# Kernel tuning notes

Measured on AMD Instinct MI355X. Metric: run time of the kernel, lower is better.

Reference implementation:

```python
import jax, jax.numpy as jnp
import numpy as np

C = 256      # d_model
H = 8        # nhead
DF = 1024    # dim_feedforward
LE = 2048    # ego tokens
LA = 2048    # other-agent tokens
N_MATCH = 1024


def setup_inputs() -> dict:
    key = jax.random.key(0)
    ks = jax.random.split(key, 16)
    def rn(k, shape, s=0.02):
        return jax.random.normal(k, shape, dtype=jnp.float32) * s
    inp = {}
    inp['x_ego'] = jax.random.normal(ks[0], (LE, C), dtype=jnp.float32)
    inp['x_agent'] = jax.random.normal(ks[1], (LA, C), dtype=jnp.float32)
    # query_fusion MLP(2C -> C -> C -> C), torch Linear weight is (out, in)
    inp['Wf1'] = rn(ks[2], (C, 2 * C)); inp['bf1'] = jnp.zeros((C,), jnp.float32)
    inp['Wf2'] = rn(ks[3], (C, C));     inp['bf2'] = jnp.zeros((C,), jnp.float32)
    inp['Wf3'] = rn(ks[4], (C, C));     inp['bf3'] = jnp.zeros((C,), jnp.float32)
    # nn.MultiheadAttention packed in-proj and out-proj
    inp['Wqkv'] = rn(ks[5], (3 * C, C)); inp['bqkv'] = jnp.zeros((3 * C,), jnp.float32)
    inp['Wo'] = rn(ks[6], (C, C));       inp['bo'] = jnp.zeros((C,), jnp.float32)
    # FFN
    inp['W1'] = rn(ks[7], (DF, C)); inp['b1'] = jnp.zeros((DF,), jnp.float32)
    inp['W2'] = rn(ks[8], (C, DF)); inp['b2'] = jnp.zeros((C,), jnp.float32)
    # LayerNorms
    inp['g1'] = jnp.ones((C,), jnp.float32); inp['be1'] = jnp.zeros((C,), jnp.float32)
    inp['g2'] = jnp.ones((C,), jnp.float32); inp['be2'] = jnp.zeros((C,), jnp.float32)
    # unique 1D positions: first N_MATCH agent positions overlap ego, rest don't
    inp['pos_ego'] = jnp.arange(LE, dtype=jnp.int32)
    pa = np.concatenate([np.arange(N_MATCH), np.arange(LA - N_MATCH) + 10_000_000])
    inp['pos_agent'] = jnp.asarray(pa, dtype=jnp.int32)
    inp['n_remain'] = LA - N_MATCH  # static python int
    return inp


def _ln(t, g, b):
    m = t.mean(-1, keepdims=True)
    v = t.var(-1, keepdims=True)
    return (t - m) / jnp.sqrt(v + 1e-5) * g + b


def reference(x_ego, x_agent, Wf1, bf1, Wf2, bf2, Wf3, bf3, Wqkv, bqkv, Wo, bo,
              W1, b1, W2, b2, g1, be1, g2, be2, pos_ego, pos_agent, n_remain):
    # ---- position-keyed grouping / fuse (replaces the host-side dict loop) ----
    eq = pos_agent[:, None] == pos_ego[None, :]          # [La, Le]
    matched_e = eq.any(axis=0)                           # ego token has same-pos agent token
    agent_for_ego = jnp.argmax(eq, axis=0)               # [Le] matching agent index (valid where matched)
    fused_in = jnp.concatenate([x_ego, x_agent[agent_for_ego]], axis=-1)  # [Le, 2C]
    h = jax.nn.relu(fused_in @ Wf1.T + bf1)
    h = jax.nn.relu(h @ Wf2.T + bf2)
    fused = h @ Wf3.T + bf3                              # query_fusion MLP output [Le, C]
    ego_out = jnp.where(matched_e[:, None], fused, x_ego)
    # agent tokens with no ego match, in original agent order (fixed count n_remain)
    remain_idx = jnp.nonzero(~eq.any(axis=1), size=n_remain)[0]
    q = jnp.concatenate([ego_out, x_agent[remain_idx]], axis=0)[None]  # (1, Lq, C)
    kv = jnp.concatenate([x_ego, x_agent], axis=0)[None]               # (1, Lk, C)
    # ---- MultiheadAttention (batch_first, eval: dropout off) ----
    Wq, Wk, Wv = jnp.split(Wqkv, 3, axis=0)
    bq, bk, bv = jnp.split(bqkv, 3, axis=0)
    dh = C // H
    def heads(t, W, b):
        return (t @ W.T + b).reshape(1, -1, H, dh).transpose(0, 2, 1, 3)
    qh, kh, vh = heads(q, Wq, bq), heads(kv, Wk, bk), heads(kv, Wv, bv)
    scores = jnp.einsum('bhqd,bhkd->bhqk', qh, kh) / (float(dh) ** 0.5)
    attn = jax.nn.softmax(scores, axis=-1)
    o = jnp.einsum('bhqk,bhkd->bhqd', attn, vh).transpose(0, 2, 1, 3).reshape(1, -1, C)
    o = o @ Wo.T + bo
    # ---- residual + norm1 + FFN + residual + norm2 ----
    yq = _ln(q + o, g1, be1)
    ff = jax.nn.relu(yq @ W1.T + b1) @ W2.T + b2
    return _ln(yq + ff, g2, be2)
```

## Files before the change

### kernel.cpp

```cpp
#include <hip/hip_runtime.h>


#define LE 2048
#define LA 2048
#define CDIM 256
#define HN 8
#define DH 32
#define DFF 1024
#define NREM 1024
#define LQC 3072
#define LKC 4096
#define KSPLIT 8
#define NIT (LKC / KSPLIT / 64)

typedef unsigned short u16;
typedef unsigned int u32;
typedef __attribute__((ext_vector_type(8))) short bf16x8;
typedef __attribute__((ext_vector_type(4))) float f32x4;

__device__ __forceinline__ u32 pk_bf16(float a, float b) {
    u32 ua = (__builtin_bit_cast(u32, a) + 0x8000u) >> 16;
    u32 ub = (__builtin_bit_cast(u32, b) + 0x8000u) >> 16;
    return ua | (ub << 16);
}
__device__ __forceinline__ u16 bf16_1(float a) {
    return (u16)((__builtin_bit_cast(u32, a) + 0x8000u) >> 16);
}
__device__ __forceinline__ float fast_exp2(float x) {
    return __builtin_amdgcn_exp2f(x);
}

__global__ __launch_bounds__(1024) void k_match(const int* __restrict__ pos_ego,
                                                const int* __restrict__ pos_agent,
                                                int* __restrict__ afe,
                                                int* __restrict__ matched,
                                                int* __restrict__ unmatched) {
    __shared__ int keyA[4096], valA[4096], keyE[4096];
    const int t = threadIdx.x;
#pragma unroll
    for (int i = 0; i < 4; ++i) { keyA[t + i * 1024] = -1; keyE[t + i * 1024] = -1; }
    __syncthreads();
#pragma unroll
    for (int i = 0; i < 2; ++i) {
        int a = t + i * 1024;
        int p = pos_agent[a];
        u32 h = ((u32)p * 2654435761u) >> 20;
        while (true) {
            int prev = atomicCAS(&keyA[h], -1, p);
            if (prev == -1) { valA[h] = a; break; }
            h = (h + 1) & 4095;
        }
        int e = t + i * 1024;
        int pe = pos_ego[e];
        u32 he = ((u32)pe * 2654435761u) >> 20;
        while (true) {
            int prev = atomicCAS(&keyE[he], -1, pe);
            if (prev == -1) break;
            he = (he + 1) & 4095;
        }
    }
    __syncthreads();
#pragma unroll
    for (int i = 0; i < 2; ++i) {
        int e = t + i * 1024;
        int p = pos_ego[e];
        u32 h = ((u32)p * 2654435761u) >> 20;
        int idx = 0, fnd = 0;
        while (true) {
            int k = keyA[h];
            if (k == p) { idx = valA[h]; fnd = 1; break; }
            if (k == -1) break;
            h = (h + 1) & 4095;
        }
        afe[e] = idx;
        matched[e] = fnd;
        int a = t + i * 1024;
        int pa_ = pos_agent[a];
        u32 ha = ((u32)pa_ * 2654435761u) >> 20;
        int fnd2 = 0;
        while (true) {
            int k = keyE[ha];
            if (k == pa_) { fnd2 = 1; break; }
            if (k == -1) break;
            ha = (ha + 1) & 4095;
        }
        unmatched[a] = !fnd2;
    }
}

struct WPtrs { const float* p[7]; };
__constant__ __device__ const int woff[8] = {0, 131072, 196608, 262144,
                                             458752, 524288, 786432, 1048576};

__global__ __launch_bounds__(256) void k_stage2(const int* __restrict__ unmatched,
                                                int* __restrict__ remain,
                                                const int* __restrict__ afe,
                                                const float* __restrict__ x_ego,
                                                const float* __restrict__ x_agent,
                                                u16* __restrict__ fused_b,
                                                WPtrs wp, u16* __restrict__ wb,
                                                u16* __restrict__ kv_b) {
    int b = blockIdx.x;
    if (b == 0) {
        __shared__ int s[256];
        int t = threadIdx.x;
        int base_i = t * 8;
        int flags[8];
        int cnt = 0;
#pragma unroll
        for (int j = 0; j < 8; ++j) { flags[j] = unmatched[base_i + j]; cnt += flags[j]; }
        s[t] = cnt;
        __syncthreads();
        for (int off = 1; off < 256; off <<= 1) {
            int v = (t >= off) ? s[t - off] : 0;
            __syncthreads();
            s[t] += v;
            __syncthreads();
        }
        int pos = s[t] - cnt;
#pragma unroll
        for (int j = 0; j < 8; ++j) {
            if (flags[j]) {
                if (pos < NREM) remain[pos] = base_i + j;
                pos++;
            }
        }
    } else if (b <= 512) {
        int t = (b - 1) * 256 + threadIdx.x;
        int e = t >> 6, c8 = t & 63;
        const float* src;
        int col;
        if (c8 < 32) { src = x_ego + (size_t)e * CDIM; col = c8 * 8; }
        else { src = x_agent + (size_t)afe[e] * CDIM; col = (c8 - 32) * 8; }
        float4 f0 = *(const float4*)(src + col);
        float4 f1 = *(const float4*)(src + col + 4);
        uint4 o;
        o.x = pk_bf16(f0.x, f0.y); o.y = pk_bf16(f0.z, f0.w);
        o.z = pk_bf16(f1.x, f1.y); o.w = pk_bf16(f1.z, f1.w);
        *(uint4*)(fused_b + (size_t)e * 512 + c8 * 8) = o;
    } else if (b <= 1024) {
        int g = ((b - 513) * 256 + threadIdx.x) * 8;
        int s = 0;
#pragma unroll
        for (int i = 1; i < 7; ++i) s += (g >= woff[i]);
        const float* src = wp.p[s] + (g - woff[s]);
        float4 f0 = *(const float4*)(src);
        float4 f1 = *(const float4*)(src + 4);
        uint4 o;
        o.x = pk_bf16(f0.x, f0.y); o.y = pk_bf16(f0.z, f0.w);
        o.z = pk_bf16(f1.x, f1.y); o.w = pk_bf16(f1.z, f1.w);
        *(uint4*)(wb + g) = o;
    } else {
        int t = (b - 1025) * 256 + threadIdx.x;
        int j = t >> 5, c8 = t & 31;
        const float* src = (j < LE) ? (x_ego + (size_t)j * CDIM)
                                    : (x_agent + (size_t)(j - LE) * CDIM);
        float4 f0 = *(const float4*)(src + c8 * 8);
        float4 f1 = *(const float4*)(src + c8 * 8 + 4);
        uint4 o;
        o.x = pk_bf16(f0.x, f0.y); o.y = pk_bf16(f0.z, f0.w);
        o.z = pk_bf16(f1.x, f1.y); o.w = pk_bf16(f1.z, f1.w);
        *(uint4*)(kv_b + (size_t)j * CDIM + c8 * 8) = o;
    }
}

template <int EPI, bool RELU>
__global__ __launch_bounds__(256) void gemm_bf16(const u16* __restrict__ A,
                                                 const u16* __restrict__ B,
                                                 const float* __restrict__ bias,
                                                 void* __restrict__ C,
                                                 int M, int N, int K) {
    const int tid = threadIdx.x;
    const int w = tid >> 6, lane = tid & 63;
    const int quad = lane >> 4, qi = lane & 15;
    const int wm = w >> 1, wn = w & 1;
    const int bm = blockIdx.y * 64, bn = blockIdx.x * 64;

    const u16* pa0 = A + (size_t)(bm + wm * 32 + qi) * K + quad * 8;
    const u16* pa1 = pa0 + (size_t)16 * K;
    const u16* pb0 = B + (size_t)(bn + wn * 32 + qi) * K + quad * 8;
    const u16* pb1 = pb0 + (size_t)16 * K;

    f32x4 acc00 = {0.f, 0.f, 0.f, 0.f}, acc01 = {0.f, 0.f, 0.f, 0.f};
    f32x4 acc10 = {0.f, 0.f, 0.f, 0.f}, acc11 = {0.f, 0.f, 0.f, 0.f};

#pragma unroll 4
    for (int k = 0; k < K; k += 32) {
        bf16x8 a0 = *(const bf16x8*)(pa0 + k);
        bf16x8 a1 = *(const bf16x8*)(pa1 + k);
        bf16x8 b0 = *(const bf16x8*)(pb0 + k);
        bf16x8 b1 = *(const bf16x8*)(pb1 + k);
        acc00 = __builtin_amdgcn_mfma_f32_16x16x32_bf16(a0, b0, acc00, 0, 0, 0);
        acc01 = __builtin_amdgcn_mfma_f32_16x16x32_bf16(a0, b1, acc01, 0, 0, 0);
        acc10 = __builtin_amdgcn_mfma_f32_16x16x32_bf16(a1, b0, acc10, 0, 0, 0);
        acc11 = __builtin_amdgcn_mfma_f32_16x16x32_bf16(a1, b1, acc11, 0, 0, 0);
    }

#pragma unroll
    for (int i = 0; i < 2; ++i) {
#pragma unroll
        for (int j = 0; j < 2; ++j) {
            f32x4 acc = (i == 0) ? (j == 0 ? acc00 : acc01) : (j == 0 ? acc10 : acc11);
            int n = bn + wn * 32 + j * 16 + qi;
            int mbase = bm + wm * 32 + i * 16 + quad * 4;
            float bs = bias[n];
            float v[4];
#pragma unroll
            for (int r = 0; r < 4; ++r) {
                float x = acc[r] + bs;
                if (RELU) x = fmaxf(x, 0.f);
                v[r] = x;
            }
            if (EPI == 0) {
                float* Cf = (float*)C;
#pragma unroll
                for (int r = 0; r < 4; ++r) Cf[(size_t)(mbase + r) * N + n] = v[r];
            } else {
                u16* Cb = (u16*)C;
#pragma unroll
                for (int r = 0; r < 4; ++r) Cb[(size_t)(mbase + r) * N + n] = bf16_1(v[r]);
            }
        }
    }
}

__global__ __launch_bounds__(256) void k_mlp3f(const u16* __restrict__ h2_b,
                                               const u16* __restrict__ Wf3_b,
                                               const float* __restrict__ bf3,
                                               const int* __restrict__ matched,
                                               const int* __restrict__ remain,
                                               const float* __restrict__ x_ego,
                                               const float* __restrict__ x_agent,
                                               float* __restrict__ qbuf,
                                               u16* __restrict__ qbuf_b) {
    const int tid = threadIdx.x;
    const int bn = blockIdx.x * 64, bm = blockIdx.y * 64;
    if (bm >= LE) {
        int row = bm + (tid >> 2);
        int col = bn + (tid & 3) * 16;
        int idx = remain[row - LE];
        idx = min(max(idx, 0), LA - 1);
        const float* src = x_agent + (size_t)idx * CDIM + col;
        float* dq = qbuf + (size_t)row * CDIM + col;
        u16* db = qbuf_b + (size_t)row * CDIM + col;
#pragma unroll
        for (int i = 0; i < 4; ++i) {
            float4 v = *(const float4*)(src + i * 4);
            *(float4*)(dq + i * 4) = v;
            *(uint2*)(db + i * 4) = make_uint2(pk_bf16(v.x, v.y), pk_bf16(v.z, v.w));
        }
        return;
    }
    const int w = tid >> 6, lane = tid & 63;
    const int quad = lane >> 4, qi = lane & 15;
    const int wm = w >> 1, wn = w & 1;
    const u16* pa0 = h2_b + (size_t)(bm + wm * 32 + qi) * 256 + quad * 8;
    const u16* pa1 = pa0 + (size_t)16 * 256;
    const u16* pb0 = Wf3_b + (size_t)(bn + wn * 32 + qi) * 256 + quad * 8;
    const u16* pb1 = pb0 + (size_t)16 * 256;
    f32x4 a00 = {0, 0, 0, 0}, a01 = {0, 0, 0, 0}, a10 = {0, 0, 0, 0}, a11 = {0, 0, 0, 0};
#pragma unroll 4
    for (int k = 0; k < 256; k += 32) {
        bf16x8 x0 = *(const bf16x8*)(pa0 + k);
        bf16x8 x1 = *(const bf16x8*)(pa1 + k);
        bf16x8 y0 = *(const bf16x8*)(pb0 + k);
        bf16x8 y1 = *(const bf16x8*)(pb1 + k);
        a00 = __builtin_amdgcn_mfma_f32_16x16x32_bf16(x0, y0, a00, 0, 0, 0);
        a01 = __builtin_amdgcn_mfma_f32_16x16x32_bf16(x0, y1, a01, 0, 0, 0);
        a10 = __builtin_amdgcn_mfma_f32_16x16x32_bf16(x1, y0, a10, 0, 0, 0);
        a11 = __builtin_amdgcn_mfma_f32_16x16x32_bf16(x1, y1, a11, 0, 0, 0);
    }
#pragma unroll
    for (int i = 0; i < 2; ++i)
#pragma unroll
        for (int jj = 0; jj < 2; ++jj) {
            f32x4 acc = (i == 0) ? (jj == 0 ? a00 : a01) : (jj == 0 ? a10 : a11);
            int n = bn + wn * 32 + jj * 16 + qi;
            int mb = bm + wm * 32 + i * 16 + quad * 4;
            float bs = bf3[n];
#pragma unroll
            for (int r = 0; r < 4; ++r) {
                int row = mb + r;
                float v = acc[r] + bs;
                if (!matched[row]) v = x_ego[(size_t)row * CDIM + n];
                qbuf[(size_t)row * CDIM + n] = v;
                qbuf_b[(size_t)row * CDIM + n] = bf16_1(v);
            }
        }
}

__global__ __launch_bounds__(256) void k_qkv(const u16* __restrict__ qbuf_b,
                                             const u16* __restrict__ kv_b,
                                             const u16* __restrict__ Wq,
                                             const u16* __restrict__ Wkv,
                                             const float* __restrict__ bqkv,
                                             u16* __restrict__ qb,
                                             u16* __restrict__ kbp,
                                             u16* __restrict__ vtb,
                                             float qscale) {
    int b = blockIdx.x;
    const u16 *A, *B;
    const float* bias;
    int bm, bn, mode;
    if (b < 192) {
        A = qbuf_b; B = Wq; bias = bqkv;
        bm = (b >> 2) * 64; bn = (b & 3) * 64; mode = 0;
    } else {
        int c = b - 192;
        A = kv_b; B = Wkv; bias = bqkv + 256;
        bm = (c >> 3) * 64; bn = (c & 7) * 64; mode = 1;
    }
    const int tid = threadIdx.x;
    const int w = tid >> 6, lane = tid & 63;
    const int quad = lane >> 4, qi = lane & 15;
    const int wm = w >> 1, wn = w & 1;
    const int K = 256;

    const u16* pa0 = A + (size_t)(bm + wm * 32 + qi) * K + quad * 8;
    const u16* pa1 = pa0 + (size_t)16 * K;
    const u16* pb0 = B + (size_t)(bn + wn * 32 + qi) * K + quad * 8;
    const u16* pb1 = pb0 + (size_t)16 * K;

    f32x4 acc00 = {0.f, 0.f, 0.f, 0.f}, acc01 = {0.f, 0.f, 0.f, 0.f};
    f32x4 acc10 = {0.f, 0.f, 0.f, 0.f}, acc11 = {0.f, 0.f, 0.f, 0.f};
#pragma unroll 4
    for (int k = 0; k < 256; k += 32) {
        bf16x8 a0 = *(const bf16x8*)(pa0 + k);
        bf16x8 a1 = *(const bf16x8*)(pa1 + k);
        bf16x8 b0 = *(const bf16x8*)(pb0 + k);
        bf16x8 b1 = *(const bf16x8*)(pb1 + k);
        acc00 = __builtin_amdgcn_mfma_f32_16x16x32_bf16(a0, b0, acc00, 0, 0, 0);
        acc01 = __builtin_amdgcn_mfma_f32_16x16x32_bf16(a0, b1, acc01, 0, 0, 0);
        acc10 = __builtin_amdgcn_mfma_f32_16x16x32_bf16(a1, b0, acc10, 0, 0, 0);
        acc11 = __builtin_amdgcn_mfma_f32_16x16x32_bf16(a1, b1, acc11, 0, 0, 0);
    }
#pragma unroll
    for (int i = 0; i < 2; ++i) {
#pragma unroll
        for (int j = 0; j < 2; ++j) {
            f32x4 acc = (i == 0) ? (j == 0 ? acc00 : acc01) : (j == 0 ? acc10 : acc11);
            int n = bn + wn * 32 + j * 16 + qi;
            int mbase = bm + wm * 32 + i * 16 + quad * 4;
            float bs = bias[n];
            float v[4];
#pragma unroll
            for (int r = 0; r < 4; ++r) v[r] = acc[r] + bs;
            if (mode == 0) {
#pragma unroll
                for (int r = 0; r < 4; ++r)
                    qb[(size_t)(mbase + r) * 256 + n] = bf16_1(v[r] * qscale);
            } else if (n < 256) {
#pragma unroll
                for (int r = 0; r < 4; ++r)
                    kbp[(size_t)(mbase + r) * 256 + n] = bf16_1(v[r]);
            } else {
                ushort4 o4;
                o4.x = bf16_1(v[0]); o4.y = bf16_1(v[1]);
                o4.z = bf16_1(v[2]); o4.w = bf16_1(v[3]);
                *(ushort4*)(vtb + (size_t)(n - 256) * LKC + mbase) = o4;
            }
        }
    }
}

__global__ __launch_bounds__(256) void attn_mfma(const u16* __restrict__ qb,
                                                 const u16* __restrict__ kb,
                                                 const u16* __restrict__ vtb,
                                                 float* __restrict__ Pl,
                                                 float* __restrict__ Pacc) {
    __shared__ u16 Kt[2][64 * 32];
    __shared__ u16 Vt[2][32 * 64];
    __shared__ u16 plds[4][16 * 64];
    const int tid = threadIdx.x;
    const int w = tid >> 6, lane = tid & 63;
    const int quad = lane >> 4, qi = lane & 15;
    const int h = blockIdx.y, ks = blockIdx.z;
    const int q0 = blockIdx.x * 64 + w * 16;

    bf16x8 qf = *(const bf16x8*)(qb + (size_t)(q0 + qi) * CDIM + h * DH + quad * 8);

    f32x4 O0 = {0.f, 0.f, 0.f, 0.f}, O1 = {0.f, 0.f, 0.f, 0.f};
    float lsum = 0.f;

    const int krow = w * 16 + (lane >> 2), kcp = lane & 3;
    const int kc = kcp ^ (krow & 3);
    const u16* kg0 = kb + (size_t)krow * CDIM + h * DH + kc * 8;
    const int kdst = krow * 32 + kcp * 8;
    const int vd = w * 8 + (lane >> 3), vcp = lane & 7;
    const int vc = vcp ^ (vd & 7);
    const u16* vg0 = vtb + (size_t)(h * DH + vd) * LKC + vc * 8;
    const int vdst = vd * 64 + vcp * 8;

    const int ka0 = qi * 32 + ((quad ^ (qi & 3)) << 3);
    const int v00o = qi * 64 + ((quad ^ (qi & 7)) << 3);
    const int v01o = qi * 64 + (((quad + 4) ^ (qi & 7)) << 3);
    const int swz = (qi & 7);
    const int rd0 = qi * 64 + ((quad ^ swz) << 3);
    const int rd1 = qi * 64 + (((4 + quad) ^ swz) << 3);
    const int half = (quad & 1) << 2;

    int kt = ks * (LKC / KSPLIT);
    {
        bf16x8 kr = *(const bf16x8*)(kg0 + (size_t)kt * CDIM);
        bf16x8 vr = *(const bf16x8*)(vg0 + kt);
        *(bf16x8*)&Kt[0][kdst] = kr;
        *(bf16x8*)&Vt[0][vdst] = vr;
    }
    int buf = 0;
    for (int it = 0; it < NIT; ++it, kt += 64) {
        __syncthreads();
        bf16x8 knext, vnext;
        const bool more = (it + 1 < NIT);
        if (more) {
            knext = *(const bf16x8*)(kg0 + (size_t)(kt + 64) * CDIM);
            vnext = *(const bf16x8*)(vg0 + kt + 64);
        }

        bf16x8 a0 = *(const bf16x8*)&Kt[buf][ka0];
        bf16x8 a1 = *(const bf16x8*)&Kt[buf][ka0 + 16 * 32];
        bf16x8 a2 = *(const bf16x8*)&Kt[buf][ka0 + 32 * 32];
        bf16x8 a3 = *(const bf16x8*)&Kt[buf][ka0 + 48 * 32];
        f32x4 z = {0.f, 0.f, 0.f, 0.f};
        f32x4 s0 = __builtin_amdgcn_mfma_f32_16x16x32_bf16(a0, qf, z, 0, 0, 0);
        f32x4 s1 = __builtin_amdgcn_mfma_f32_16x16x32_bf16(a1, qf, z, 0, 0, 0);
        f32x4 s2 = __builtin_amdgcn_mfma_f32_16x16x32_bf16(a2, qf, z, 0, 0, 0);
        f32x4 s3 = __builtin_amdgcn_mfma_f32_16x16x32_bf16(a3, qf, z, 0, 0, 0);

        float p0[4], p1[4], p2[4], p3[4];
#pragma unroll
        for (int r = 0; r < 4; ++r) {
            p0[r] = fast_exp2(s0[r]); p1[r] = fast_exp2(s1[r]);
            p2[r] = fast_exp2(s2[r]); p3[r] = fast_exp2(s3[r]);
            lsum += p0[r] + p1[r] + p2[r] + p3[r];
        }

        u16* pb = &plds[w][0];
#pragma unroll
        for (int t2 = 0; t2 < 4; ++t2) {
            int jg = t2 * 2 + (quad >> 1);
            int off = qi * 64 + ((jg ^ swz) << 3) + half;
            uint2 pw;
            float* pp = (t2 == 0) ? p0 : (t2 == 1) ? p1 : (t2 == 2) ? p2 : p3;
            pw.x = pk_bf16(pp[0], pp[1]);
            pw.y = pk_bf16(pp[2], pp[3]);
            *(uint2*)&pb[off] = pw;
        }
        bf16x8 pa0 = *(bf16x8*)&pb[rd0];
        bf16x8 pa1 = *(bf16x8*)&pb[rd1];

        bf16x8 v00 = *(const bf16x8*)&Vt[buf][v00o];
        bf16x8 v01 = *(const bf16x8*)&Vt[buf][v01o];
        bf16x8 v10 = *(const bf16x8*)&Vt[buf][v00o + 16 * 64];
        bf16x8 v11 = *(const bf16x8*)&Vt[buf][v01o + 16 * 64];
        O0 = __builtin_amdgcn_mfma_f32_16x16x32_bf16(pa0, v00, O0, 0, 0, 0);
        O0 = __builtin_amdgcn_mfma_f32_16x16x32_bf16(pa1, v01, O0, 0, 0, 0);
        O1 = __builtin_amdgcn_mfma_f32_16x16x32_bf16(pa0, v10, O1, 0, 0, 0);
        O1 = __builtin_amdgcn_mfma_f32_16x16x32_bf16(pa1, v11, O1, 0, 0, 0);

        if (more) {
            *(bf16x8*)&Kt[buf ^ 1][kdst] = knext;
            *(bf16x8*)&Vt[buf ^ 1][vdst] = vnext;
        }
        buf ^= 1;
    }

    lsum += __shfl_xor(lsum, 16, 64);
    lsum += __shfl_xor(lsum, 32, 64);

    int pbase = (h * KSPLIT + ks) * LQC + q0;
    if (quad == 0) Pl[pbase + qi] = lsum;
#pragma unroll
    for (int r = 0; r < 4; ++r) {
        int q = quad * 4 + r;
        float* pa = Pacc + (size_t)(pbase + q) * 32;
        pa[qi] = O0[r];
        pa[16 + qi] = O1[r];
    }
}

__global__ __launch_bounds__(256) void attn_combine(const float* __restrict__ Pl,
                                                    const float* __restrict__ Pacc,
                                                    u16* __restrict__ attn_b) {
    int t = blockIdx.x * 256 + threadIdx.x;
    int row = t >> 6;
    int h = (t >> 3) & 7;
    int d4 = t & 7;
    float L = 0.f;
    float o[4] = {};
#pragma unroll
    for (int ck = 0; ck < KSPLIT; ++ck) {
        size_t pidx = (size_t)(h * KSPLIT + ck) * LQC + row;
        L += Pl[pidx];
        float4 a = *(const float4*)(Pacc + pidx * 32 + d4 * 4);
        o[0] += a.x; o[1] += a.y; o[2] += a.z; o[3] += a.w;
    }
    float inv = 1.0f / L;
    ushort4 ov;
    ov.x = bf16_1(o[0] * inv); ov.y = bf16_1(o[1] * inv);
    ov.z = bf16_1(o[2] * inv); ov.w = bf16_1(o[3] * inv);
    *(ushort4*)(attn_b + (size_t)row * CDIM + h * DH + d4 * 4) = ov;
}

template <bool EMIT_BF16>
__global__ __launch_bounds__(256) void ln_kernel(const float* __restrict__ X,
                                                 const float* __restrict__ R,
                                                 const float* __restrict__ g,
                                                 const float* __restrict__ b,
                                                 float* __restrict__ out,
                                                 u16* __restrict__ out_b) {
    int lane = threadIdx.x & 63;
    int row = blockIdx.x * 4 + (threadIdx.x >> 6);
    const float* x = X + (size_t)row * CDIM;
    const float* r = R + (size_t)row * CDIM;
    float4 xv = *(const float4*)(x + lane * 4);
    float4 rv = *(const float4*)(r + lane * 4);
    float v[4] = {xv.x + rv.x, xv.y + rv.y, xv.z + rv.z, xv.w + rv.w};
    float s = v[0] + v[1] + v[2] + v[3];
    float sq = v[0] * v[0] + v[1] * v[1] + v[2] * v[2] + v[3] * v[3];
#pragma unroll
    for (int off = 32; off >= 1; off >>= 1) {
        s += __shfl_xor(s, off, 64);
        sq += __shfl_xor(sq, off, 64);
    }
    float mean = s * (1.f / 256.f);
    float var = sq * (1.f / 256.f) - mean * mean;
    float rstd = rsqrtf(var + 1e-5f);
    float4 gv = *(const float4*)(g + lane * 4);
    float4 bv = *(const float4*)(b + lane * 4);
    float4 o = make_float4((v[0] - mean) * rstd * gv.x + bv.x,
                           (v[1] - mean) * rstd * gv.y + bv.y,
                           (v[2] - mean) * rstd * gv.z + bv.z,
                           (v[3] - mean) * rstd * gv.w + bv.w);
    *(float4*)(out + (size_t)row * CDIM + lane * 4) = o;
    if (EMIT_BF16) {
        uint2 ob;
        ob.x = pk_bf16(o.x, o.y);
        ob.y = pk_bf16(o.z, o.w);
        *(uint2*)(out_b + (size_t)row * CDIM + lane * 4) = ob;
    }
}

extern "C" void kernel_launch(void* const* d_in, const int* in_sizes, int n_in,
                              void* d_out, int out_size, void* d_ws, size_t ws_size,
                              hipStream_t stream) {
    const float* x_ego = (const float*)d_in[0];
    const float* x_agent = (const float*)d_in[1];
    const float* Wf1 = (const float*)d_in[2];
    const float* bf1 = (const float*)d_in[3];
    const float* Wf2 = (const float*)d_in[4];
    const float* bf2 = (const float*)d_in[5];
    const float* Wf3 = (const float*)d_in[6];
    const float* bf3 = (const float*)d_in[7];
    const float* Wqkv = (const float*)d_in[8];
    const float* bqkv = (const float*)d_in[9];
    const float* Wo = (const float*)d_in[10];
    const float* bo = (const float*)d_in[11];
    const float* W1 = (const float*)d_in[12];
    const float* b1 = (const float*)d_in[13];
    const float* W2 = (const float*)d_in[14];
    const float* b2 = (const float*)d_in[15];
    const float* g1 = (const float*)d_in[16];
    const float* be1 = (const float*)d_in[17];
    const float* g2 = (const float*)d_in[18];
    const float* be2 = (const float*)d_in[19];
    const int* pos_ego = (const int*)d_in[20];
    const int* pos_agent = (const int*)d_in[21];

    float* ws = (float*)d_ws;
    size_t o = 0;
    float* qbuf = ws + o; o += 786432;
    float* o2 = ws + o; o += 786432;
    float* yq = ws + o; o += 786432;
    float* ff2 = o2;
    float* Pl = ws + o; o += HN * KSPLIT * LQC;
    float* Pacc = ws + o; o += (size_t)HN * KSPLIT * LQC * 32;
    u16* wb = (u16*)(ws + o); o += 524288;
    u16* fused_b = (u16*)(ws + o); o += 524288;
    u16* h1_b = (u16*)(ws + o); o += 262144;
    u16* h2_b = (u16*)(ws + o); o += 262144;
    u16* qbuf_b = (u16*)(ws + o); o += 393216;
    u16* kv_b = (u16*)(ws + o); o += 524288;
    u16* qb = (u16*)(ws + o); o += 393216;
    u16* kb = (u16*)(ws + o); o += 524288;
    u16* vtb = (u16*)(ws + o); o += 524288;
    u16* attn_b = (u16*)(ws + o); o += 393216;
    u16* ff1_b = (u16*)(ws + o); o += 1572864;
    u16* yq_b = (u16*)(ws + o); o += 393216;
    int* afe = (int*)(ws + o);
    int* matched = afe + LE;
    int* unmatched = matched + LE;
    int* remain = unmatched + LA;

    const u16* Wf1_b = wb + 0;
    const u16* Wf2_b = wb + 131072;
    const u16* Wf3_b = wb + 196608;
    const u16* Wq_b = wb + 262144;
    const u16* Wkv_b = wb + 327680;
    const u16* Wo_b = wb + 458752;
    const u16* W1_b = wb + 524288;
    const u16* W2_b = wb + 786432;

    k_match<<<1, 1024, 0, stream>>>(pos_ego, pos_agent, afe, matched, unmatched);
    WPtrs wp;
    wp.p[0] = Wf1; wp.p[1] = Wf2; wp.p[2] = Wf3; wp.p[3] = Wqkv;
    wp.p[4] = Wo; wp.p[5] = W1; wp.p[6] = W2;
    k_stage2<<<1537, 256, 0, stream>>>(unmatched, remain, afe, x_ego, x_agent,
                                       fused_b, wp, wb, kv_b);

    const float qscale = 0.17677669529663687f * 1.4426950408889634f;

    gemm_bf16<1, true><<<dim3(4, 32), 256, 0, stream>>>(fused_b, Wf1_b, bf1, h1_b,
                                                        LE, 256, 512);
    gemm_bf16<1, true><<<dim3(4, 32), 256, 0, stream>>>(h1_b, Wf2_b, bf2, h2_b,
                                                        LE, 256, 256);
    k_mlp3f<<<dim3(4, 48), 256, 0, stream>>>(h2_b, Wf3_b, bf3, matched, remain,
                                             x_ego, x_agent, qbuf, qbuf_b);

    k_qkv<<<704, 256, 0, stream>>>(qbuf_b, kv_b, Wq_b, Wkv_b, bqkv, qb, kb, vtb, qscale);

    attn_mfma<<<dim3(LQC / 64, HN, KSPLIT), 256, 0, stream>>>(qb, kb, vtb, Pl, Pacc);
    attn_combine<<<(LQC * 64) / 256, 256, 0, stream>>>(Pl, Pacc, attn_b);

    gemm_bf16<0, false><<<dim3(4, 48), 256, 0, stream>>>(attn_b, Wo_b, bo, o2,
                                                         LQC, 256, 256);
    ln_kernel<true><<<LQC / 4, 256, 0, stream>>>(qbuf, o2, g1, be1, yq, yq_b);

    gemm_bf16<1, true><<<dim3(16, 48), 256, 0, stream>>>(yq_b, W1_b, b1, ff1_b,
                                                         LQC, DFF, 256);
    gemm_bf16<0, false><<<dim3(4, 48), 256, 0, stream>>>(ff1_b, W2_b, b2, ff2,
                                                         LQC, 256, DFF);
    ln_kernel<false><<<LQC / 4, 256, 0, stream>>>(yq, ff2, g2, be2, (float*)d_out, nullptr);
}
```

Measured before the change: 220.2 us.

## Merge prep kernels, fuse gather into MLP1, XCD-swizzle tiles, fp16 attention partials

Merges the hash-match kernel and the conversion/scan kernel into one k_prep launch. The scan now runs over 1024 threads from shared memory. A new k_mlp1 gathers x_ego/x_agent rows and converts them to bf16 directly in the A-operand load, which removes the fused_b buffer and its separate pass. GEMM, QKV and attention blocks are remapped so consecutive tiles go to the same XCD for L2 locality. Split-K attention partial outputs are stored as fp16 instead of fp32, halving that traffic at some precision cost.

```diff
diff --git a/kernel.cpp b/kernel.cpp
--- a/kernel.cpp
+++ b/kernel.cpp
@@ -29,117 +29,108 @@
 __device__ __forceinline__ float fast_exp2(float x) {
     return __builtin_amdgcn_exp2f(x);
 }
-
-__global__ __launch_bounds__(1024) void k_match(const int* __restrict__ pos_ego,
-                                                const int* __restrict__ pos_agent,
-                                                int* __restrict__ afe,
-                                                int* __restrict__ matched,
-                                                int* __restrict__ unmatched) {
-    __shared__ int keyA[4096], valA[4096], keyE[4096];
-    const int t = threadIdx.x;
-#pragma unroll
-    for (int i = 0; i < 4; ++i) { keyA[t + i * 1024] = -1; keyE[t + i * 1024] = -1; }
-    __syncthreads();
-#pragma unroll
-    for (int i = 0; i < 2; ++i) {
-        int a = t + i * 1024;
-        int p = pos_agent[a];
-        u32 h = ((u32)p * 2654435761u) >> 20;
-        while (true) {
-            int prev = atomicCAS(&keyA[h], -1, p);
-            if (prev == -1) { valA[h] = a; break; }
-            h = (h + 1) & 4095;
-        }
-        int e = t + i * 1024;
-        int pe = pos_ego[e];
-        u32 he = ((u32)pe * 2654435761u) >> 20;
-        while (true) {
-            int prev = atomicCAS(&keyE[he], -1, pe);
-            if (prev == -1) break;
-            he = (he + 1) & 4095;
-        }
-    }
-    __syncthreads();
-#pragma unroll
-    for (int i = 0; i < 2; ++i) {
-        int e = t + i * 1024;
-        int p = pos_ego[e];
-        u32 h = ((u32)p * 2654435761u) >> 20;
-        int idx = 0, fnd = 0;
-        while (true) {
-            int k = keyA[h];
-            if (k == p) { idx = valA[h]; fnd = 1; break; }
-            if (k == -1) break;
-            h = (h + 1) & 4095;
-        }
-        afe[e] = idx;
-        matched[e] = fnd;
-        int a = t + i * 1024;
-        int pa_ = pos_agent[a];
-        u32 ha = ((u32)pa_ * 2654435761u) >> 20;
-        int fnd2 = 0;
-        while (true) {
-            int k = keyE[ha];
-            if (k == pa_) { fnd2 = 1; break; }
-            if (k == -1) break;
-            ha = (ha + 1) & 4095;
-        }
-        unmatched[a] = !fnd2;
-    }
+__device__ __forceinline__ bf16x8 ld_pack8(const float* p) {
+    float4 f0 = *(const float4*)p;
+    float4 f1 = *(const float4*)(p + 4);
+    union { u32 u[4]; bf16x8 v; } o;
+    o.u[0] = pk_bf16(f0.x, f0.y); o.u[1] = pk_bf16(f0.z, f0.w);
+    o.u[2] = pk_bf16(f1.x, f1.y); o.u[3] = pk_bf16(f1.z, f1.w);
+    return o.v;
+}
+
+__device__ __forceinline__ void xcd_tile(int& bm, int& bn) {
+    int gx = gridDim.x;
+    int tot = gx * gridDim.y;
+    int p = blockIdx.y * gx + blockIdx.x;
+    int l = p;
+    if (!(tot & 7)) { int c = p & 7, s = p >> 3; l = c * (tot >> 3) + s; }
+    bm = (l / gx) * 64;
+    bn = (l % gx) * 64;
 }
 
 struct WPtrs { const float* p[7]; };
 __constant__ __device__ const int woff[8] = {0, 131072, 196608, 262144,
                                              458752, 524288, 786432, 1048576};
 
-__global__ __launch_bounds__(256) void k_stage2(const int* __restrict__ unmatched,
-                                                int* __restrict__ remain,
-                                                const int* __restrict__ afe,
-                                                const float* __restrict__ x_ego,
-                                                const float* __restrict__ x_agent,
-                                                u16* __restrict__ fused_b,
-                                                WPtrs wp, u16* __restrict__ wb,
-                                                u16* __restrict__ kv_b) {
-    int b = blockIdx.x;
+__global__ __launch_bounds__(1024) void k_prep(const int* __restrict__ pos_ego,
+                                               const int* __restrict__ pos_agent,
+                                               int* __restrict__ afe,
+                                               int* __restrict__ matched,
+                                               int* __restrict__ remain,
+                                               const float* __restrict__ x_ego,
+                                               const float* __restrict__ x_agent,
+                                               WPtrs wp, u16* __restrict__ wb,
+                                               u16* __restrict__ kv_b) {
+    const int b = blockIdx.x;
+    const int t = threadIdx.x;
     if (b == 0) {
-        __shared__ int s[256];
-        int t = threadIdx.x;
-        int base_i = t * 8;
-        int flags[8];
-        int cnt = 0;
-#pragma unroll
-        for (int j = 0; j < 8; ++j) { flags[j] = unmatched[base_i + j]; cnt += flags[j]; }
-        s[t] = cnt;
+        __shared__ int keyA[4096], valA[4096], keyE[4096];
+        __shared__ int unm[2048];
+#pragma unroll
+        for (int i = 0; i < 4; ++i) { keyA[t + i * 1024] = -1; keyE[t + i * 1024] = -1; }
         __syncthreads();
-        for (int off = 1; off < 256; off <<= 1) {
-            int v = (t >= off) ? s[t - off] : 0;
+#pragma unroll
+        for (int i = 0; i < 2; ++i) {
+            int a = t + i * 1024;
+            int p = pos_agent[a];
+            u32 h = ((u32)p * 2654435761u) >> 20;
+            while (true) {
+                int prev = atomicCAS(&keyA[h], -1, p);
+                if (prev == -1) { valA[h] = a; break; }
+                h = (h + 1) & 4095;
+            }
+            int e = t + i * 1024;
+            int pe = pos_ego[e];
+            u32 he = ((u32)pe * 2654435761u) >> 20;
+            while (true) {
+                int prev = atomicCAS(&keyE[he], -1, pe);
+                if (prev == -1) break;
+                he = (he + 1) & 4095;
+            }
+        }
+        __syncthreads();
+#pragma unroll
+        for (int i = 0; i < 2; ++i) {
+            int e = t + i * 1024;
+            int p = pos_ego[e];
+            u32 h = ((u32)p * 2654435761u) >> 20;
+            int idx = 0, fnd = 0;
+            while (true) {
+                int k = keyA[h];
+                if (k == p) { idx = valA[h]; fnd = 1; break; }
+                if (k == -1) break;
+                h = (h + 1) & 4095;
+            }
+            afe[e] = idx;
+            matched[e] = fnd;
+            int a = t + i * 1024;
+            int pa_ = pos_agent[a];
+            u32 ha = ((u32)pa_ * 2654435761u) >> 20;
+            int fnd2 = 0;
+            while (true) {
+                int k = keyE[ha];
+                if (k == pa_) { fnd2 = 1; break; }
+                if (k == -1) break;
+                ha = (ha + 1) & 4095;
+            }
+            unm[a] = !fnd2;
+        }
+        __syncthreads();
+        int f0 = unm[2 * t], f1 = unm[2 * t + 1];
+        int cnt = f0 + f1;
+        valA[t] = cnt;
+        __syncthreads();
+        for (int off = 1; off < 1024; off <<= 1) {
+            int v = (t >= off) ? valA[t - off] : 0;
             __syncthreads();
-            s[t] += v;
+            valA[t] += v;
             __syncthreads();
         }
-        int pos = s[t] - cnt;
-#pragma unroll
-        for (int j = 0; j < 8; ++j) {
-            if (flags[j]) {
-                if (pos < NREM) remain[pos] = base_i + j;
-                pos++;
-            }
-        }
-    } else if (b <= 512) {
-        int t = (b - 1) * 256 + threadIdx.x;
-        int e = t >> 6, c8 = t & 63;
-        const float* src;
-        int col;
-        if (c8 < 32) { src = x_ego + (size_t)e * CDIM; col = c8 * 8; }
-        else { src = x_agent + (size_t)afe[e] * CDIM; col = (c8 - 32) * 8; }
-        float4 f0 = *(const float4*)(src + col);
-        float4 f1 = *(const float4*)(src + col + 4);
-        uint4 o;
-        o.x = pk_bf16(f0.x, f0.y); o.y = pk_bf16(f0.z, f0.w);
-        o.z = pk_bf16(f1.x, f1.y); o.w = pk_bf16(f1.z, f1.w);
-        *(uint4*)(fused_b + (size_t)e * 512 + c8 * 8) = o;
-    } else if (b <= 1024) {
-        int g = ((b - 513) * 256 + threadIdx.x) * 8;
+        int pos = valA[t] - cnt;
+        if (f0 && pos < NREM) remain[pos] = 2 * t;
+        if (f1 && pos + f0 < NREM) remain[pos + f0] = 2 * t + 1;
+    } else if (b <= 128) {
+        int g = ((b - 1) * 1024 + t) * 8;
         int s = 0;
 #pragma unroll
         for (int i = 1; i < 7; ++i) s += (g >= woff[i]);
@@ -151,8 +142,8 @@
         o.z = pk_bf16(f1.x, f1.y); o.w = pk_bf16(f1.z, f1.w);
         *(uint4*)(wb + g) = o;
     } else {
-        int t = (b - 1025) * 256 + threadIdx.x;
-        int j = t >> 5, c8 = t & 31;
+        int tt = (b - 129) * 1024 + t;
+        int j = tt >> 5, c8 = tt & 31;
         const float* src = (j < LE) ? (x_ego + (size_t)j * CDIM)
                                     : (x_agent + (size_t)(j - LE) * CDIM);
         float4 f0 = *(const float4*)(src + c8 * 8);
@@ -174,7 +165,8 @@
     const int w = tid >> 6, lane = tid & 63;
     const int quad = lane >> 4, qi = lane & 15;
     const int wm = w >> 1, wn = w & 1;
-    const int bm = blockIdx.y * 64, bn = blockIdx.x * 64;
+    int bm, bn;
+    xcd_tile(bm, bn);
 
     const u16* pa0 = A + (size_t)(bm + wm * 32 + qi) * K + quad * 8;
     const u16* pa1 = pa0 + (size_t)16 * K;
@@ -224,6 +216,68 @@
     }
 }
 
+__global__ __launch_bounds__(256) void k_mlp1(const float* __restrict__ x_ego,
+                                              const float* __restrict__ x_agent,
+                                              const int* __restrict__ afe,
+                                              const u16* __restrict__ Wf1_b,
+                                              const float* __restrict__ bf1,
+                                              u16* __restrict__ h1_b) {
+    const int tid = threadIdx.x;
+    const int w = tid >> 6, lane = tid & 63;
+    const int quad = lane >> 4, qi = lane & 15;
+    const int wm = w >> 1, wn = w & 1;
+    int bm, bn;
+    xcd_tile(bm, bn);
+
+    const int r0 = bm + wm * 32 + qi, r1 = r0 + 16;
+    const float* pe0 = x_ego + (size_t)r0 * CDIM + quad * 8;
+    const float* pe1 = x_ego + (size_t)r1 * CDIM + quad * 8;
+    const float* pg0 = x_agent + (size_t)afe[r0] * CDIM + quad * 8;
+    const float* pg1 = x_agent + (size_t)afe[r1] * CDIM + quad * 8;
+    const u16* pb0 = Wf1_b + (size_t)(bn + wn * 32 + qi) * 512 + quad * 8;
+    const u16* pb1 = pb0 + (size_t)16 * 512;
+
+    f32x4 acc00 = {0.f, 0.f, 0.f, 0.f}, acc01 = {0.f, 0.f, 0.f, 0.f};
+    f32x4 acc10 = {0.f, 0.f, 0.f, 0.f}, acc11 = {0.f, 0.f, 0.f, 0.f};
+
+#pragma unroll 4
+    for (int k = 0; k < 256; k += 32) {
+        bf16x8 a0 = ld_pack8(pe0 + k);
+        bf16x8 a1 = ld_pack8(pe1 + k);
+        bf16x8 b0 = *(const bf16x8*)(pb0 + k);
+        bf16x8 b1 = *(const bf16x8*)(pb1 + k);
+        acc00 = __builtin_amdgcn_mfma_f32_16x16x32_bf16(a0, b0, acc00, 0, 0, 0);
+        acc01 = __builtin_amdgcn_mfma_f32_16x16x32_bf16(a0, b1, acc01, 0, 0, 0);
+        acc10 = __builtin_amdgcn_mfma_f32_16x16x32_bf16(a1, b0, acc10, 0, 0, 0);
+        acc11 = __builtin_amdgcn_mfma_f32_16x16x32_bf16(a1, b1, acc11, 0, 0, 0);
+    }
+#pragma unroll 4
+    for (int k = 0; k < 256; k += 32) {
+        bf16x8 a0 = ld_pack8(pg0 + k);
+        bf16x8 a1 = ld_pack8(pg1 + k);
+        bf16x8 b0 = *(const bf16x8*)(pb0 + 256 + k);
+        bf16x8 b1 = *(const bf16x8*)(pb1 + 256 + k);
+        acc00 = __builtin_amdgcn_mfma_f32_16x16x32_bf16(a0, b0, acc00, 0, 0, 0);
+        acc01 = __builtin_amdgcn_mfma_f32_16x16x32_bf16(a0, b1, acc01, 0, 0, 0);
+        acc10 = __builtin_amdgcn_mfma_f32_16x16x32_bf16(a1, b0, acc10, 0, 0, 0);
+        acc11 = __builtin_amdgcn_mfma_f32_16x16x32_bf16(a1, b1, acc11, 0, 0, 0);
+    }
+#pragma unroll
+    for (int i = 0; i < 2; ++i)
+#pragma unroll
+        for (int j = 0; j < 2; ++j) {
+            f32x4 acc = (i == 0) ? (j == 0 ? acc00 : acc01) : (j == 0 ? acc10 : acc11);
+            int n = bn + wn * 32 + j * 16 + qi;
+            int mbase = bm + wm * 32 + i * 16 + quad * 4;
+            float bs = bf1[n];
+#pragma unroll
+            for (int r = 0; r < 4; ++r) {
+                float x = fmaxf(acc[r] + bs, 0.f);
+                h1_b[(size_t)(mbase + r) * 256 + n] = bf16_1(x);
+            }
+        }
+}
+
 __global__ __launch_bounds__(256) void k_mlp3f(const u16* __restrict__ h2_b,
                                                const u16* __restrict__ Wf3_b,
                                                const float* __restrict__ bf3,
@@ -234,7 +288,8 @@
                                                float* __restrict__ qbuf,
                                                u16* __restrict__ qbuf_b) {
     const int tid = threadIdx.x;
-    const int bn = blockIdx.x * 64, bm = blockIdx.y * 64;
+    int bm, bn;
+    xcd_tile(bm, bn);
     if (bm >= LE) {
         int row = bm + (tid >> 2);
         int col = bn + (tid & 3) * 16;
@@ -298,7 +353,12 @@
                                              u16* __restrict__ kbp,
                                              u16* __restrict__ vtb,
                                              float qscale) {
-    int b = blockIdx.x;
+    int b;
+    {
+        int p = blockIdx.x;
+        int c = p & 7, s = p >> 3;
+        b = c * 88 + s;
+    }
     const u16 *A, *B;
     const float* bias;
     int bm, bn, mode;
@@ -367,15 +427,23 @@
                                                  const u16* __restrict__ kb,
                                                  const u16* __restrict__ vtb,
                                                  float* __restrict__ Pl,
-                                                 float* __restrict__ Pacc) {
+                                                 u16* __restrict__ Pacc) {
     __shared__ u16 Kt[2][64 * 32];
     __shared__ u16 Vt[2][32 * 64];
     __shared__ u16 plds[4][16 * 64];
     const int tid = threadIdx.x;
     const int w = tid >> 6, lane = tid & 63;
     const int quad = lane >> 4, qi = lane & 15;
-    const int h = blockIdx.y, ks = blockIdx.z;
-    const int q0 = blockIdx.x * 64 + w * 16;
+    int h, ks, q0;
+    {
+        int p = (blockIdx.z * gridDim.y + blockIdx.y) * gridDim.x + blockIdx.x;
+        int c = p & 7, s = p >> 3;
+        int l = c * 384 + s;
+        int qblk = l % 48;
+        int hk = l / 48;
+        h = hk & 7; ks = hk >> 3;
+        q0 = qblk * 64 + w * 16;
+    }
 
     bf16x8 qf = *(const bf16x8*)(qb + (size_t)(q0 + qi) * CDIM + h * DH + quad * 8);
 
@@ -472,14 +540,14 @@
 #pragma unroll
     for (int r = 0; r < 4; ++r) {
         int q = quad * 4 + r;
-        float* pa = Pacc + (size_t)(pbase + q) * 32;
-        pa[qi] = O0[r];
-        pa[16 + qi] = O1[r];
+        u16* pa = Pacc + (size_t)(pbase + q) * 32;
+        pa[qi] = __builtin_bit_cast(u16, (_Float16)O0[r]);
+        pa[16 + qi] = __builtin_bit_cast(u16, (_Float16)O1[r]);
     }
 }
 
 __global__ __launch_bounds__(256) void attn_combine(const float* __restrict__ Pl,
-                                                    const float* __restrict__ Pacc,
+                                                    const u16* __restrict__ Pacc,
                                                     u16* __restrict__ attn_b) {
     int t = blockIdx.x * 256 + threadIdx.x;
     int row = t >> 6;
@@ -491,8 +559,11 @@
     for (int ck = 0; ck < KSPLIT; ++ck) {
         size_t pidx = (size_t)(h * KSPLIT + ck) * LQC + row;
         L += Pl[pidx];
-        float4 a = *(const float4*)(Pacc + pidx * 32 + d4 * 4);
-        o[0] += a.x; o[1] += a.y; o[2] += a.z; o[3] += a.w;
+        ushort4 a = *(const ushort4*)(Pacc + pidx * 32 + d4 * 4);
+        o[0] += (float)__builtin_bit_cast(_Float16, a.x);
+        o[1] += (float)__builtin_bit_cast(_Float16, a.y);
+        o[2] += (float)__builtin_bit_cast(_Float16, a.z);
+        o[3] += (float)__builtin_bit_cast(_Float16, a.w);
     }
     float inv = 1.0f / L;
     ushort4 ov;
@@ -573,9 +644,8 @@
     float* yq = ws + o; o += 786432;
     float* ff2 = o2;
     float* Pl = ws + o; o += HN * KSPLIT * LQC;
-    float* Pacc = ws + o; o += (size_t)HN * KSPLIT * LQC * 32;
+    u16* Pacc = (u16*)(ws + o); o += (size_t)HN * KSPLIT * LQC * 16;
     u16* wb = (u16*)(ws + o); o += 524288;
-    u16* fused_b = (u16*)(ws + o); o += 524288;
     u16* h1_b = (u16*)(ws + o); o += 262144;
     u16* h2_b = (u16*)(ws + o); o += 262144;
     u16* qbuf_b = (u16*)(ws + o); o += 393216;
@@ -588,8 +658,7 @@
     u16* yq_b = (u16*)(ws + o); o += 393216;
     int* afe = (int*)(ws + o);
     int* matched = afe + LE;
-    int* unmatched = matched + LE;
-    int* remain = unmatched + LA;
+    int* remain = matched + LE;
 
     const u16* Wf1_b = wb + 0;
     const u16* Wf2_b = wb + 131072;
@@ -600,17 +669,16 @@
     const u16* W1_b = wb + 524288;
     const u16* W2_b = wb + 786432;
 
-    k_match<<<1, 1024, 0, stream>>>(pos_ego, pos_agent, afe, matched, unmatched);
     WPtrs wp;
     wp.p[0] = Wf1; wp.p[1] = Wf2; wp.p[2] = Wf3; wp.p[3] = Wqkv;
     wp.p[4] = Wo; wp.p[5] = W1; wp.p[6] = W2;
-    k_stage2<<<1537, 256, 0, stream>>>(unmatched, remain, afe, x_ego, x_agent,
-                                       fused_b, wp, wb, kv_b);
+
+    k_prep<<<257, 1024, 0, stream>>>(pos_ego, pos_agent, afe, matched, remain,
+                                     x_ego, x_agent, wp, wb, kv_b);
 
     const float qscale = 0.17677669529663687f * 1.4426950408889634f;
 
-    gemm_bf16<1, true><<<dim3(4, 32), 256, 0, stream>>>(fused_b, Wf1_b, bf1, h1_b,
-                                                        LE, 256, 512);
+    k_mlp1<<<dim3(4, 32), 256, 0, stream>>>(x_ego, x_agent, afe, Wf1_b, bf1, h1_b);
     gemm_bf16<1, true><<<dim3(4, 32), 256, 0, stream>>>(h1_b, Wf2_b, bf2, h2_b,
                                                         LE, 256, 256);
     k_mlp3f<<<dim3(4, 48), 256, 0, stream>>>(h2_b, Wf3_b, bf3, matched, remain,
```

Measured after the change: 221.4 us. Within noise of the previous version (+0.6%).
